# Kernel tuning notes

Hardware: AMD Instinct MI355X
Metric: run time of the kernel (lower is better)

The kernel has to match this reference:

```python
import jax, jax.numpy as jnp
import numpy as np

NUM_TOPICS = 100
VOCAB = 8192
MC_N = 20
MD_N = 20
LAMBDA_D = 0.7
LAMBDA_A = 100.0
WARMUP_RATIO = 0.5
NUM_EPOCHS = 200


def setup_inputs() -> dict:
    key = jax.random.key(0)
    k1, k2 = jax.random.split(key)
    beta = jax.random.normal(k1, (NUM_TOPICS, VOCAB), dtype=jnp.float32)
    W = jax.random.uniform(k2, (VOCAB, VOCAB), dtype=jnp.float32)
    # fill_diagonal_(1) in __init__
    d = jnp.arange(VOCAB)
    W = W.at[d, d].set(1.0)
    return {"beta": beta, "coherence_weight": W, "epoch": 120}


def reference(beta, coherence_weight, epoch):
    K, V = beta.shape
    rows = jnp.arange(K)[:, None]

    # --- Mc: top-Mc_n mask -> additive -99999 on non-topk entries ---
    _, mc_idx = jax.lax.top_k(beta, MC_N)                      # [K, Mc_n]
    Mc = jnp.zeros_like(beta).at[rows, mc_idx].set(1.0)        # [K, V]
    Mc_add = (1.0 - Mc) * (-99999.0)

    # softmax over masked beta is detached in the original
    p = jax.lax.stop_gradient(jax.nn.softmax(beta + Mc_add, axis=1))
    M = p @ coherence_weight                                    # [K, V]

    # row-wise min-max normalize, then Wc = 1 - normalized
    m_min = jnp.min(M, axis=1, keepdims=True)
    m_max = jnp.max(M, axis=1, keepdims=True)
    Wc = 1.0 - (M - m_min) / (m_max - m_min)

    loss = 100.0 * jax.nn.softmax(beta, axis=1) ** 2 * Wc       # [K, V]

    # --- diversity mask Md (lambda_d > 0.5 branch) ---
    _, md_idx = jax.lax.top_k(beta, MD_N)
    Md_mask = jnp.zeros_like(beta).at[rows, md_idx].set(1.0)    # [K, V]
    # Md[t, v] = any other row has v in its top-Md_n
    col_sum = jnp.sum(Md_mask, axis=0)                          # [V]
    Md = (col_sum[None, :] - Md_mask) > 0                       # [K, V] bool

    pos = jnp.sum(jnp.where(Md, loss, 0.0))
    neg = jnp.sum(jnp.where(Md, 0.0, loss))
    total = (pos * LAMBDA_D + neg * (1.0 - LAMBDA_D)) * 2.0

    warmup_epochs = int(WARMUP_RATIO * NUM_EPOCHS)              # 100
    lambda_a_delta = LAMBDA_A / warmup_epochs
    lambda_a = epoch * lambda_a_delta if epoch < warmup_epochs else LAMBDA_A
    return lambda_a * total
```

## Files before the change

### kernel.cpp

```cpp
#include <hip/hip_runtime.h>
#include <math.h>

#define NT 100
#define VOCAB 8192
#define TOPN 20
#define NWV 4
#define WCOLS 2048
#define SCAP 256

__global__ __launch_bounds__(256) void topk_kernel(
    const float* __restrict__ beta,
    int*   __restrict__ top_idx,
    float* __restrict__ top_p,
    float* __restrict__ rowstats,
    float* __restrict__ out)
{
    const int k = blockIdx.x;
    const int t = threadIdx.x;
    const int wv = t >> 6;
    const int lane = t & 63;
    if (k == 0 && t == 0) *out = 0.f;

    __shared__ float cu[NWV * SCAP];
    __shared__ int   cid[NWV * SCAP];
    __shared__ float smaxs[NWV], ssums[NWV];
    __shared__ float pv[NWV * TOPN];
    __shared__ int   pid[NWV * TOPN];
    __shared__ float s_winv[TOPN];
    __shared__ int   s_wini[TOPN];
    __shared__ float s_ps, s_rowmax;

    const float* base = beta + (size_t)k * VOCAB + wv * WCOLS;
    float4 r[8];
    float mx = -INFINITY;
#pragma unroll
    for (int i = 0; i < 8; ++i) {
        r[i] = *reinterpret_cast<const float4*>(base + (size_t)(i * 64 + lane) * 4);
        mx = fmaxf(mx, fmaxf(fmaxf(r[i].x, r[i].y), fmaxf(r[i].z, r[i].w)));
    }
#pragma unroll
    for (int off = 32; off >= 1; off >>= 1) mx = fmaxf(mx, __shfl_xor(mx, off));
    const float smax = mx;

    float se = 0.f;
#pragma unroll
    for (int i = 0; i < 8; ++i) {
        se += expf(r[i].x - smax) + expf(r[i].y - smax)
            + expf(r[i].z - smax) + expf(r[i].w - smax);
    }
#pragma unroll
    for (int off = 32; off >= 1; off >>= 1) se += __shfl_xor(se, off);
    const float ssum = se;

    if (lane == 0) { smaxs[wv] = smax; ssums[wv] = ssum; }

    float T = smax - 1.5f;
    for (int g = 0; g < 16; ++g) {
        int c = 0;
#pragma unroll
        for (int i = 0; i < 8; ++i) {
            c += (r[i].x >= T) + (r[i].y >= T) + (r[i].z >= T) + (r[i].w >= T);
        }
#pragma unroll
        for (int off = 32; off >= 1; off >>= 1) c += __shfl_xor(c, off);
        if (c >= TOPN) break;
        T -= 0.4f;
    }

    int wbase = 0;
#pragma unroll
    for (int i = 0; i < 8; ++i) {
#pragma unroll
        for (int e = 0; e < 4; ++e) {
            const float v = (&r[i].x)[e];
            const bool pr = (v >= T);
            const unsigned long long mask = __ballot(pr);
            const int pre = __popcll(mask & ((1ull << lane) - 1ull));
            if (pr) {
                const int p = wbase + pre;
                if (p < SCAP) {
                    cu[wv * SCAP + p]  = v;
                    cid[wv * SCAP + p] = wv * WCOLS + (i * 64 + lane) * 4 + e;
                }
            }
            wbase += __popcll(mask);
        }
    }
    const int n = min(wbase, SCAP);

    for (int it = 0; it < TOPN; ++it) {
        float bv = -INFINITY; int bp = -1;
        for (int p = lane; p < n; p += 64) {
            const float v = cu[wv * SCAP + p];
            if (v > bv) { bv = v; bp = p; }
        }
#pragma unroll
        for (int off = 32; off >= 1; off >>= 1) {
            const float ov = __shfl_down(bv, off);
            const int   op = __shfl_down(bp, off);
            if (ov > bv) { bv = ov; bp = op; }
        }
        bp = __shfl(bp, 0);
        bv = __shfl(bv, 0);
        if (lane == 0) {
            pv[wv * TOPN + it]  = bv;
            pid[wv * TOPN + it] = (bp >= 0) ? cid[wv * SCAP + bp] : 0;
        }
        if (bp >= 0) cu[wv * SCAP + bp] = -INFINITY;
    }
    __syncthreads();

    if (wv == 0) {
        for (int it = 0; it < TOPN; ++it) {
            float bv = -INFINITY; int bp = -1;
            for (int p = lane; p < NWV * TOPN; p += 64) {
                const float v = pv[p];
                if (v > bv) { bv = v; bp = p; }
            }
#pragma unroll
            for (int off = 32; off >= 1; off >>= 1) {
                const float ov = __shfl_down(bv, off);
                const int   op = __shfl_down(bp, off);
                if (ov > bv) { bv = ov; bp = op; }
            }
            bp = __shfl(bp, 0);
            bv = __shfl(bv, 0);
            if (lane == 0) { s_winv[it] = bv; s_wini[it] = pid[bp]; }
            pv[bp] = -INFINITY;
        }
        if (lane == 0) {
            const float rowmax = s_winv[0];
            float ps = 0.f;
#pragma unroll
            for (int j = 0; j < TOPN; ++j) ps += expf(s_winv[j] - rowmax);
            float rs = 0.f;
#pragma unroll
            for (int s = 0; s < NWV; ++s) rs += ssums[s] * expf(smaxs[s] - rowmax);
            s_rowmax = rowmax;
            s_ps = ps;
            rowstats[2 * k + 0] = rowmax;
            rowstats[2 * k + 1] = rs;
        }
    }
    __syncthreads();
    if (t < TOPN) {
        top_idx[k * TOPN + t] = s_wini[t];
        top_p[k * TOPN + t]   = expf(s_winv[t] - s_rowmax) / s_ps;
    }
}

__global__ __launch_bounds__(1024) void fused_kernel(
    const float* __restrict__ beta,
    const float* __restrict__ W,
    const int*   __restrict__ top_idx,
    const float* __restrict__ top_p,
    const float* __restrict__ rowstats,
    const int*   __restrict__ epoch,
    float* __restrict__ out)
{
    const int k = blockIdx.x;
    const int t = threadIdx.x;

    __shared__ int   cnt[VOCAB];
    __shared__ int   sIdx[TOPN];
    __shared__ float sP[TOPN];
    __shared__ float sA[16], sB[16], sC[16], sD[16], sE[16], sF[16];

    if (t < TOPN) { sIdx[t] = top_idx[k * TOPN + t]; sP[t] = top_p[k * TOPN + t]; }
#pragma unroll
    for (int i = 0; i < VOCAB / 1024; ++i) cnt[i * 1024 + t] = 0;
    __syncthreads();

#pragma unroll 2
    for (int e = t; e < NT * TOPN; e += 1024) atomicAdd(&cnt[top_idx[e]], 1);
    if (t < TOPN) atomicSub(&cnt[sIdx[t]], 1);

    int   idx_r[TOPN];
    float p_r[TOPN];
#pragma unroll
    for (int j = 0; j < TOPN; ++j) { idx_r[j] = sIdx[j]; p_r[j] = sP[j]; }

    const float rmax = rowstats[2 * k + 0];
    const float rinv = 1.0f / rowstats[2 * k + 1];

    __syncthreads();

    float mn = INFINITY, mxv = -INFINITY;
    float Apos = 0.f, Bpos = 0.f, Aneg = 0.f, Bneg = 0.f;

#pragma unroll
    for (int seg = 0; seg < 2; ++seg) {
        const int col = seg * 4096 + t * 4;

        float4 m = make_float4(0.f, 0.f, 0.f, 0.f);
#pragma unroll
        for (int j = 0; j < TOPN; ++j) {
            const float4 w = *reinterpret_cast<const float4*>(W + (size_t)idx_r[j] * VOCAB + col);
            const float pj = p_r[j];
            m.x += pj * w.x; m.y += pj * w.y; m.z += pj * w.z; m.w += pj * w.w;
        }
        mn  = fminf(mn,  fminf(fminf(m.x, m.y), fminf(m.z, m.w)));
        mxv = fmaxf(mxv, fmaxf(fmaxf(m.x, m.y), fmaxf(m.z, m.w)));

        const float4 bv = *reinterpret_cast<const float4*>(beta + (size_t)k * VOCAB + col);
        float4 w4;
        w4.x = expf(bv.x - rmax) * rinv;  w4.x = 100.f * w4.x * w4.x;
        w4.y = expf(bv.y - rmax) * rinv;  w4.y = 100.f * w4.y * w4.y;
        w4.z = expf(bv.z - rmax) * rinv;  w4.z = 100.f * w4.z * w4.z;
        w4.w = expf(bv.w - rmax) * rinv;  w4.w = 100.f * w4.w * w4.w;

        const int4 c4 = *reinterpret_cast<const int4*>(cnt + col);
        if (c4.x > 0) { Apos += w4.x; Bpos += w4.x * m.x; } else { Aneg += w4.x; Bneg += w4.x * m.x; }
        if (c4.y > 0) { Apos += w4.y; Bpos += w4.y * m.y; } else { Aneg += w4.y; Bneg += w4.y * m.y; }
        if (c4.z > 0) { Apos += w4.z; Bpos += w4.z * m.z; } else { Aneg += w4.z; Bneg += w4.z * m.z; }
        if (c4.w > 0) { Apos += w4.w; Bpos += w4.w * m.w; } else { Aneg += w4.w; Bneg += w4.w * m.w; }
    }

#pragma unroll
    for (int off = 32; off >= 1; off >>= 1) {
        mn   = fminf(mn,  __shfl_down(mn,  off));
        mxv  = fmaxf(mxv, __shfl_down(mxv, off));
        Apos += __shfl_down(Apos, off);
        Bpos += __shfl_down(Bpos, off);
        Aneg += __shfl_down(Aneg, off);
        Bneg += __shfl_down(Bneg, off);
    }
    if ((t & 63) == 0) {
        const int w = t >> 6;
        sA[w] = mn; sB[w] = mxv; sC[w] = Apos; sD[w] = Bpos; sE[w] = Aneg; sF[w] = Bneg;
    }
    __syncthreads();
    if (t == 0) {
        float a = sA[0], b = sB[0], Ap = 0.f, Bp = 0.f, An = 0.f, Bn = 0.f;
#pragma unroll
        for (int w = 0; w < 16; ++w) {
            a  = fminf(a, sA[w]);
            b  = fmaxf(b, sB[w]);
            Ap += sC[w]; Bp += sD[w]; An += sE[w]; Bn += sF[w];
        }
        const float inv = 1.0f / (b - a);
        const float pos = Ap - inv * (Bp - a * Ap);
        const float neg = An - inv * (Bn - a * An);
        const int e = *epoch;
        const float la = (e < 100) ? (float)e : 100.0f;
        atomicAdd(out, la * (pos * 0.7f + neg * 0.3f) * 2.0f);
    }
}

extern "C" void kernel_launch(void* const* d_in, const int* in_sizes, int n_in,
                              void* d_out, int out_size, void* d_ws, size_t ws_size,
                              hipStream_t stream)
{
    (void)in_sizes; (void)n_in; (void)out_size; (void)ws_size;
    const float* beta  = (const float*)d_in[0];
    const float* W     = (const float*)d_in[1];
    const int*   epoch = (const int*)d_in[2];
    float* out = (float*)d_out;

    char* ws = (char*)d_ws;
    int*   top_idx  = (int*)ws;    ws += NT * TOPN * sizeof(int);
    float* top_p    = (float*)ws;  ws += NT * TOPN * sizeof(float);
    float* rowstats = (float*)ws;  ws += NT * 2 * sizeof(float);

    topk_kernel<<<NT, 256, 0, stream>>>(beta, top_idx, top_p, rowstats, out);
    fused_kernel<<<NT, 1024, 0, stream>>>(beta, W, top_idx, top_p, rowstats, epoch, out);
}
```

Measured before the change: 46.47 us.

## Split each topic row across two blocks with flag-based partial combine

The fused kernel now launches two 1024-thread blocks per topic, each covering half of the vocabulary columns. This doubles the grid from 100 to 200 blocks so more of the GPU's compute units are occupied, and halves the shared-memory count array per block. Each block writes six partial statistics (min, max and weighted sums) to workspace. The second block of each pair to finish, detected through an atomic counter that the top-k kernel resets, combines both halves and adds the row's result to the output. The cost is an extra global round-trip with fences for the cross-block reduction, and every block still scans the full top-k index list to build its half of the histogram.

```diff
diff --git a/kernel.cpp b/kernel.cpp
--- a/kernel.cpp
+++ b/kernel.cpp
@@ -7,18 +7,21 @@
 #define NWV 4
 #define WCOLS 2048
 #define SCAP 256
+#define HCOLS 4096
 
 __global__ __launch_bounds__(256) void topk_kernel(
     const float* __restrict__ beta,
     int*   __restrict__ top_idx,
     float* __restrict__ top_p,
     float* __restrict__ rowstats,
+    int*   __restrict__ tflag,
     float* __restrict__ out)
 {
     const int k = blockIdx.x;
     const int t = threadIdx.x;
     const int wv = t >> 6;
     const int lane = t & 63;
+    if (t == 0) tflag[k] = 0;
     if (k == 0 && t == 0) *out = 0.f;
 
     __shared__ float cu[NWV * SCAP];
@@ -156,24 +159,36 @@
     const float* __restrict__ top_p,
     const float* __restrict__ rowstats,
     const int*   __restrict__ epoch,
+    float* __restrict__ part6,
+    int*   __restrict__ tflag,
     float* __restrict__ out)
 {
-    const int k = blockIdx.x;
+    const int b = blockIdx.x;
+    const int k = b >> 1;
+    const int h = b & 1;
     const int t = threadIdx.x;
-
-    __shared__ int   cnt[VOCAB];
+    const int lo = h * HCOLS;
+
+    __shared__ int   cnt[HCOLS];
     __shared__ int   sIdx[TOPN];
     __shared__ float sP[TOPN];
     __shared__ float sA[16], sB[16], sC[16], sD[16], sE[16], sF[16];
+    __shared__ int   s_old;
 
     if (t < TOPN) { sIdx[t] = top_idx[k * TOPN + t]; sP[t] = top_p[k * TOPN + t]; }
 #pragma unroll
-    for (int i = 0; i < VOCAB / 1024; ++i) cnt[i * 1024 + t] = 0;
+    for (int i = 0; i < HCOLS / 1024; ++i) cnt[i * 1024 + t] = 0;
     __syncthreads();
 
 #pragma unroll 2
-    for (int e = t; e < NT * TOPN; e += 1024) atomicAdd(&cnt[top_idx[e]], 1);
-    if (t < TOPN) atomicSub(&cnt[sIdx[t]], 1);
+    for (int e = t; e < NT * TOPN; e += 1024) {
+        const int v = top_idx[e] - lo;
+        if ((unsigned)v < (unsigned)HCOLS) atomicAdd(&cnt[v], 1);
+    }
+    if (t < TOPN) {
+        const int v = sIdx[t] - lo;
+        if ((unsigned)v < (unsigned)HCOLS) atomicSub(&cnt[v], 1);
+    }
 
     int   idx_r[TOPN];
     float p_r[TOPN];
@@ -185,35 +200,31 @@
 
     __syncthreads();
 
-    float mn = INFINITY, mxv = -INFINITY;
+    const int col = lo + t * 4;
+    float4 m = make_float4(0.f, 0.f, 0.f, 0.f);
+#pragma unroll
+    for (int j = 0; j < TOPN; ++j) {
+        const float4 w = *reinterpret_cast<const float4*>(W + (size_t)idx_r[j] * VOCAB + col);
+        const float pj = p_r[j];
+        m.x += pj * w.x; m.y += pj * w.y; m.z += pj * w.z; m.w += pj * w.w;
+    }
+    float mn  = fminf(fminf(m.x, m.y), fminf(m.z, m.w));
+    float mxv = fmaxf(fmaxf(m.x, m.y), fmaxf(m.z, m.w));
+
+    const float4 bv = *reinterpret_cast<const float4*>(beta + (size_t)k * VOCAB + col);
+    float4 w4;
+    w4.x = expf(bv.x - rmax) * rinv;  w4.x = 100.f * w4.x * w4.x;
+    w4.y = expf(bv.y - rmax) * rinv;  w4.y = 100.f * w4.y * w4.y;
+    w4.z = expf(bv.z - rmax) * rinv;  w4.z = 100.f * w4.z * w4.z;
+    w4.w = expf(bv.w - rmax) * rinv;  w4.w = 100.f * w4.w * w4.w;
+
     float Apos = 0.f, Bpos = 0.f, Aneg = 0.f, Bneg = 0.f;
-
-#pragma unroll
-    for (int seg = 0; seg < 2; ++seg) {
-        const int col = seg * 4096 + t * 4;
-
-        float4 m = make_float4(0.f, 0.f, 0.f, 0.f);
-#pragma unroll
-        for (int j = 0; j < TOPN; ++j) {
-            const float4 w = *reinterpret_cast<const float4*>(W + (size_t)idx_r[j] * VOCAB + col);
-            const float pj = p_r[j];
-            m.x += pj * w.x; m.y += pj * w.y; m.z += pj * w.z; m.w += pj * w.w;
-        }
-        mn  = fminf(mn,  fminf(fminf(m.x, m.y), fminf(m.z, m.w)));
-        mxv = fmaxf(mxv, fmaxf(fmaxf(m.x, m.y), fmaxf(m.z, m.w)));
-
-        const float4 bv = *reinterpret_cast<const float4*>(beta + (size_t)k * VOCAB + col);
-        float4 w4;
-        w4.x = expf(bv.x - rmax) * rinv;  w4.x = 100.f * w4.x * w4.x;
-        w4.y = expf(bv.y - rmax) * rinv;  w4.y = 100.f * w4.y * w4.y;
-        w4.z = expf(bv.z - rmax) * rinv;  w4.z = 100.f * w4.z * w4.z;
-        w4.w = expf(bv.w - rmax) * rinv;  w4.w = 100.f * w4.w * w4.w;
-
-        const int4 c4 = *reinterpret_cast<const int4*>(cnt + col);
-        if (c4.x > 0) { Apos += w4.x; Bpos += w4.x * m.x; } else { Aneg += w4.x; Bneg += w4.x * m.x; }
-        if (c4.y > 0) { Apos += w4.y; Bpos += w4.y * m.y; } else { Aneg += w4.y; Bneg += w4.y * m.y; }
-        if (c4.z > 0) { Apos += w4.z; Bpos += w4.z * m.z; } else { Aneg += w4.z; Bneg += w4.z * m.z; }
-        if (c4.w > 0) { Apos += w4.w; Bpos += w4.w * m.w; } else { Aneg += w4.w; Bneg += w4.w * m.w; }
+    {
+        const int lc = t * 4;
+        if (cnt[lc + 0] > 0) { Apos += w4.x; Bpos += w4.x * m.x; } else { Aneg += w4.x; Bneg += w4.x * m.x; }
+        if (cnt[lc + 1] > 0) { Apos += w4.y; Bpos += w4.y * m.y; } else { Aneg += w4.y; Bneg += w4.y * m.y; }
+        if (cnt[lc + 2] > 0) { Apos += w4.z; Bpos += w4.z * m.z; } else { Aneg += w4.z; Bneg += w4.z * m.z; }
+        if (cnt[lc + 3] > 0) { Apos += w4.w; Bpos += w4.w * m.w; } else { Aneg += w4.w; Bneg += w4.w * m.w; }
     }
 
 #pragma unroll
@@ -230,20 +241,36 @@
         sA[w] = mn; sB[w] = mxv; sC[w] = Apos; sD[w] = Bpos; sE[w] = Aneg; sF[w] = Bneg;
     }
     __syncthreads();
+
     if (t == 0) {
-        float a = sA[0], b = sB[0], Ap = 0.f, Bp = 0.f, An = 0.f, Bn = 0.f;
+        float a = sA[0], bb = sB[0], Ap = 0.f, Bp = 0.f, An = 0.f, Bn = 0.f;
 #pragma unroll
         for (int w = 0; w < 16; ++w) {
             a  = fminf(a, sA[w]);
-            b  = fmaxf(b, sB[w]);
+            bb = fmaxf(bb, sB[w]);
             Ap += sC[w]; Bp += sD[w]; An += sE[w]; Bn += sF[w];
         }
-        const float inv = 1.0f / (b - a);
-        const float pos = Ap - inv * (Bp - a * Ap);
-        const float neg = An - inv * (Bn - a * An);
-        const int e = *epoch;
-        const float la = (e < 100) ? (float)e : 100.0f;
-        atomicAdd(out, la * (pos * 0.7f + neg * 0.3f) * 2.0f);
+        float* p6 = part6 + (size_t)b * 6;
+        p6[0] = a; p6[1] = bb; p6[2] = Ap; p6[3] = Bp; p6[4] = An; p6[5] = Bn;
+        __threadfence();
+        s_old = atomicAdd(&tflag[k], 1);
+        if (s_old == 1) {
+            __threadfence();
+            const float* q0 = part6 + (size_t)(2 * k + 0) * 6;
+            const float* q1 = part6 + (size_t)(2 * k + 1) * 6;
+            const float gmn = fminf(q0[0], q1[0]);
+            const float gmx = fmaxf(q0[1], q1[1]);
+            const float A_p = q0[2] + q1[2];
+            const float B_p = q0[3] + q1[3];
+            const float A_n = q0[4] + q1[4];
+            const float B_n = q0[5] + q1[5];
+            const float inv = 1.0f / (gmx - gmn);
+            const float pos = A_p - inv * (B_p - gmn * A_p);
+            const float neg = A_n - inv * (B_n - gmn * A_n);
+            const int e = *epoch;
+            const float la = (e < 100) ? (float)e : 100.0f;
+            atomicAdd(out, la * (pos * 0.7f + neg * 0.3f) * 2.0f);
+        }
     }
 }
 
@@ -261,7 +288,12 @@
     int*   top_idx  = (int*)ws;    ws += NT * TOPN * sizeof(int);
     float* top_p    = (float*)ws;  ws += NT * TOPN * sizeof(float);
     float* rowstats = (float*)ws;  ws += NT * 2 * sizeof(float);
-
-    topk_kernel<<<NT, 256, 0, stream>>>(beta, top_idx, top_p, rowstats, out);
-    fused_kernel<<<NT, 1024, 0, stream>>>(beta, W, top_idx, top_p, rowstats, epoch, out);
+    ws = (char*)(((size_t)ws + 255) & ~(size_t)255);
+    float* part6    = (float*)ws;  ws += NT * 2 * 6 * sizeof(float);
+    ws = (char*)(((size_t)ws + 255) & ~(size_t)255);
+    int*   tflag    = (int*)ws;    ws += NT * 64;
+
+    topk_kernel<<<NT, 256, 0, stream>>>(beta, top_idx, top_p, rowstats, tflag, out);
+    fused_kernel<<<NT * 2, 1024, 0, stream>>>(beta, W, top_idx, top_p, rowstats,
+                                              epoch, part6, tflag, out);
 }
```

After: 49.53 us. +6.6%, slower.
